# Kernel optimization log

Hardware: AMD Instinct MI355X
Metric: run time of the kernel (lower is better)

Reference implementation:

```python
import jax, jax.numpy as jnp
import numpy as np
import math

D_MODEL = 2048
K = 64
W = 512              # window_size
STRIDE = W // 2      # = 256
EMA_ALPHA = 0.9
N_RETRIEVE = 8
EPS = 1e-12


def _build_cheby(k, w):
    # cheby_mat[k, n] = cos(k * arccos(t_n)), t_n = cos(pi*(2n+1)/(2w))
    ns = np.arange(w, dtype=np.float64)
    t = np.cos(np.pi * (2 * ns + 1) / (2 * w))
    ks = np.arange(k, dtype=np.float64)
    return jnp.asarray(np.cos(ks[:, None] * np.arccos(t)[None, :]), dtype=jnp.float32)


def setup_inputs() -> dict:
    key = jax.random.key(0)
    ks = jax.random.split(key, 5)
    B, S = 2, 8192
    scan_out = jax.random.normal(ks[0], (B, S, D_MODEL), dtype=jnp.float32)
    buf = jax.random.normal(ks[1], (W, D_MODEL), dtype=jnp.float32)  # pre-filled circular buffer
    # unit-modulus random-phase complex roles: r_k[d] = exp(i*theta)
    phases = jax.random.uniform(ks[2], (K, D_MODEL), dtype=jnp.float32) * (2.0 * math.pi)
    roles_real = jnp.cos(phases)
    roles_imag = jnp.sin(phases)
    w_bands = 1.0 / (jnp.arange(K, dtype=jnp.float32) + 1.0)  # w_init = 1/(k+1)
    retrieve_proj_w = jax.random.normal(ks[3], (D_MODEL, D_MODEL), dtype=jnp.float32) * 0.02
    inject_gate = jnp.zeros((1,), dtype=jnp.float32)
    cheby_mat = _build_cheby(K, W)
    return dict(scan_out=scan_out, buf=buf, roles_real=roles_real, roles_imag=roles_imag,
                w_bands=w_bands, retrieve_proj_w=retrieve_proj_w, inject_gate=inject_gate,
                cheby_mat=cheby_mat)


def reference(scan_out, buf, roles_real, roles_imag, w_bands, retrieve_proj_w, inject_gate, cheby_mat):
    S = scan_out.shape[1]
    h_mean = scan_out.mean(axis=0)                      # [S, D] batch-mean like torch code
    n_chunks = S // STRIDE
    chunks = h_mean.reshape(n_chunks, STRIDE, D_MODEL)  # each chunk triggers one bind

    init = (buf, jnp.int32(0),
            jnp.zeros((K, D_MODEL), jnp.float32),   # c_past
            jnp.zeros((D_MODEL,), jnp.float32),     # V_mem_real
            jnp.zeros((D_MODEL,), jnp.float32),     # V_mem_imag
            jnp.zeros((K,), jnp.float32),           # _coeff_norms (EMA)
            jnp.zeros((K,), jnp.float32))           # spectral_delta

    def step(carry, chunk):
        b, pos, c_past, vr, vi, cnorms, _ = carry
        # circular-buffer write of `stride` tokens starting at pos
        b = jax.lax.dynamic_update_slice(b, chunk, (pos, 0))
        pos = (pos + STRIDE) % W
        order = (jnp.arange(W, dtype=jnp.int32) + pos) % W   # oldest-first reorder
        data = b[order]                                      # [W, D]
        # Chebyshev coefficients: c = (2/W) * cheby_mat @ data, c0 halved
        coeffs = (2.0 / W) * (cheby_mat @ data)              # [K, D]
        coeffs = coeffs.at[0].multiply(0.5)
        # HRR-normalized bind into holographic memory via EMA
        norms = jnp.maximum(jnp.linalg.norm(coeffs, axis=-1, keepdims=True), EPS)
        cn = coeffs / norms
        cnorms = EMA_ALPHA * cnorms + (1.0 - EMA_ALPHA) * norms[:, 0]
        vr = EMA_ALPHA * vr + (1.0 - EMA_ALPHA) * (cn * roles_real).sum(axis=0)
        vi = EMA_ALPHA * vi + (1.0 - EMA_ALPHA) * (cn * roles_imag).sum(axis=0)
        # spectral delta vs previous window's coefficients
        delta = jnp.linalg.norm(coeffs - c_past, axis=-1)    # [K]
        return (b, pos, coeffs, vr, vi, cnorms, delta), None

    (b, pos, c_now, vr, vi, cnorms, delta), _ = jax.lax.scan(step, init, chunks)

    # retrieve: unbind top-J bands by spectral delta, denormalize, weight, project
    _, top = jax.lax.top_k(delta, N_RETRIEVE)                # [J]
    rr = roles_real[top]
    ri = roles_imag[top]
    retrieved = (vr[None, :] * rr + vi[None, :] * ri) * jnp.maximum(cnorms[top], EPS)[:, None]  # [J, D]
    weights = jax.nn.softplus(w_bands[top])                  # [J]
    ctx = (weights[:, None] * retrieved).sum(axis=0)         # [D]
    out = (ctx @ retrieve_proj_w.T) * jax.nn.sigmoid(inject_gate[0])  # [D]
    return out, delta, vr, vi
```

## Files before the change

### kernel.cpp

```cpp
#include <hip/hip_runtime.h>
#include <math.h>

#define D_MODEL 2048
#define KB_ 64
#define NCHUNK 32

typedef __bf16 bf16;
typedef __attribute__((ext_vector_type(8))) __bf16 bf16x8;
typedef __attribute__((ext_vector_type(4))) __bf16 bf16x4;
typedef __attribute__((ext_vector_type(4))) float f32x4;

#define OFF_COEFFS 0
#define OFF_NSQ    (32 * 64 * 2048)
#define OFF_NORMS  (OFF_NSQ + 32 * 64 * 32)
#define OFF_PARTR  (OFF_NORMS + 2048)
#define OFF_PARTI  (OFF_PARTR + 32 * 2048)
#define OFF_CTX    (OFF_PARTI + 32 * 2048)
#define OFF_CHEB2  (OFF_CTX + 2048)

__global__ __launch_bounds__(256) void k0_prep(
    const float* __restrict__ cheby, bf16* __restrict__ cheb2)
{
  int flat = blockIdx.x * 256 + threadIdx.x;
  cheb2[flat] = (bf16)cheby[flat];
}

__global__ __launch_bounds__(256) void k1_mfma(
    const float* __restrict__ scan, const float* __restrict__ buf,
    const bf16* __restrict__ cheb2, float* __restrict__ coeffs,
    float* __restrict__ nsq_part)
{
  __shared__ bf16 Bs[64 * 72];

  const int t = threadIdx.x;
  const int dt = blockIdx.x;
  const int c  = blockIdx.y;
  const int w = t >> 6, lane = t & 63;
  const int quad = lane >> 4, r16 = lane & 15;
  const int d0 = dt * 64;
  const int n0 = (t >> 4) * 4;
  const int d4 = (t & 15) * 4;
  const float* scan1 = scan + 8192 * 2048;

  f32x4 acc[4];
#pragma unroll
  for (int tn = 0; tn < 4; ++tn) acc[tn] = (f32x4){0.f, 0.f, 0.f, 0.f};

  for (int nb = 0; nb < 8; ++nb) {
    const bf16* abase = cheb2 + (w * 16 + r16) * 512 + nb * 64 + quad * 8;
    bf16x8 a0 = *(const bf16x8*)(abase);
    bf16x8 a1 = *(const bf16x8*)(abase + 32);

    float vv[4][4];
    if (c == 0 && nb < 4) {
      const float* bp = buf + (256 + nb * 64 + n0) * 2048 + d0 + d4;
#pragma unroll
      for (int i = 0; i < 4; ++i) {
        float4 v = *(const float4*)(bp + i * 2048);
        vv[i][0] = v.x; vv[i][1] = v.y; vv[i][2] = v.z; vv[i][3] = v.w;
      }
    } else {
      int gbase = (c * 256 - 256 + nb * 64 + n0) * 2048 + d0 + d4;
#pragma unroll
      for (int i = 0; i < 4; ++i) {
        float4 a = *(const float4*)(scan + gbase + i * 2048);
        float4 b = *(const float4*)(scan1 + gbase + i * 2048);
        vv[i][0] = 0.5f * (a.x + b.x); vv[i][1] = 0.5f * (a.y + b.y);
        vv[i][2] = 0.5f * (a.z + b.z); vv[i][3] = 0.5f * (a.w + b.w);
      }
    }
    __syncthreads();
#pragma unroll
    for (int x = 0; x < 4; ++x) {
      bf16x4 e = {(bf16)vv[0][x], (bf16)vv[1][x], (bf16)vv[2][x], (bf16)vv[3][x]};
      *(bf16x4*)(Bs + (d4 + x) * 72 + n0) = e;
    }
    __syncthreads();

#pragma unroll
    for (int ks = 0; ks < 2; ++ks) {
      bf16x8 a = ks ? a1 : a0;
#pragma unroll
      for (int tn = 0; tn < 4; ++tn) {
        bf16x8 bfr = *(const bf16x8*)(Bs + (tn * 16 + r16) * 72 + ks * 32 + quad * 8);
        acc[tn] = __builtin_amdgcn_mfma_f32_16x16x32_bf16(a, bfr, acc[tn], 0, 0, 0);
      }
    }
  }

  const float scale = 2.0f / 512.0f;
  float sq[4] = {0.f, 0.f, 0.f, 0.f};
#pragma unroll
  for (int tn = 0; tn < 4; ++tn) {
#pragma unroll
    for (int rr = 0; rr < 4; ++rr) {
      int band = w * 16 + quad * 4 + rr;
      float sc = (band == 0) ? scale * 0.5f : scale;
      float v = acc[tn][rr] * sc;
      coeffs[(c * 64 + band) * 2048 + d0 + tn * 16 + r16] = v;
      sq[rr] += v * v;
    }
  }
#pragma unroll
  for (int off = 8; off > 0; off >>= 1) {
#pragma unroll
    for (int rr = 0; rr < 4; ++rr) sq[rr] += __shfl_down(sq[rr], off);
  }
  if (r16 == 0) {
#pragma unroll
    for (int rr = 0; rr < 4; ++rr)
      nsq_part[(c * 64 + w * 16 + quad * 4 + rr) * 32 + dt] = sq[rr];
  }
}

__global__ __launch_bounds__(256) void kd_delta(
    const float* __restrict__ coeffs, float* __restrict__ dout)
{
  const int k = blockIdx.x, tid = threadIdx.x;
  const float* p1 = coeffs + (31 * 64 + k) * 2048;
  const float* p0 = coeffs + (30 * 64 + k) * 2048;
  float s = 0.f;
#pragma unroll
  for (int i = 0; i < 2; ++i) {
    float4 a = *(const float4*)(p1 + tid * 4 + i * 1024);
    float4 b = *(const float4*)(p0 + tid * 4 + i * 1024);
    float x = a.x - b.x, y = a.y - b.y, z = a.z - b.z, ww = a.w - b.w;
    s += x * x + y * y + z * z + ww * ww;
  }
  for (int o = 32; o > 0; o >>= 1) s += __shfl_down(s, o, 64);
  __shared__ float red[4];
  if ((tid & 63) == 0) red[tid >> 6] = s;
  __syncthreads();
  if (tid == 0) dout[D_MODEL + k] = sqrtf(red[0] + red[1] + red[2] + red[3]);
}

__global__ __launch_bounds__(256) void k3_bind(
    const float* __restrict__ coeffs, const float* __restrict__ nsq_part,
    const float* __restrict__ rr, const float* __restrict__ ri,
    float* __restrict__ part_r, float* __restrict__ part_i,
    float* __restrict__ norms)
{
  __shared__ float inv_s[64];
  const int tid = threadIdx.x;
  const int c = blockIdx.y;
  if (tid < 64) {
    float s = 0.f;
#pragma unroll
    for (int dt = 0; dt < 32; ++dt) s += nsq_part[(c * 64 + tid) * 32 + dt];
    float nrm = fmaxf(sqrtf(s), 1e-12f);
    inv_s[tid] = 1.0f / nrm;
    if (blockIdx.x == 0) norms[c * 64 + tid] = nrm;
  }
  __syncthreads();
  const int d4 = (blockIdx.x * 256 + tid) * 4;
  const float wc = 0.1f * powf(0.9f, (float)(31 - c));
  float4 ar = make_float4(0.f, 0.f, 0.f, 0.f);
  float4 ai = make_float4(0.f, 0.f, 0.f, 0.f);
  for (int k = 0; k < KB_; ++k) {
    float4 cf = *(const float4*)(coeffs + (c * 64 + k) * 2048 + d4);
    float inv = inv_s[k];
    float4 r = *(const float4*)(rr + k * D_MODEL + d4);
    float4 im = *(const float4*)(ri + k * D_MODEL + d4);
    float cx = cf.x * inv, cy = cf.y * inv, cz = cf.z * inv, cw = cf.w * inv;
    ar.x += cx * r.x; ar.y += cy * r.y; ar.z += cz * r.z; ar.w += cw * r.w;
    ai.x += cx * im.x; ai.y += cy * im.y; ai.z += cz * im.z; ai.w += cw * im.w;
  }
  *(float4*)(part_r + c * D_MODEL + d4) =
      make_float4(wc * ar.x, wc * ar.y, wc * ar.z, wc * ar.w);
  *(float4*)(part_i + c * D_MODEL + d4) =
      make_float4(wc * ai.x, wc * ai.y, wc * ai.z, wc * ai.w);
}

__global__ __launch_bounds__(256) void k4_ctx(
    const float* __restrict__ norms, const float* __restrict__ part_r,
    const float* __restrict__ part_i, const float* __restrict__ rr,
    const float* __restrict__ ri, const float* __restrict__ wbands,
    float* __restrict__ dout, float* __restrict__ ctx)
{
  __shared__ float cn_s[64];
  __shared__ int top_s[8];
  __shared__ float wgt_s[8];
  const int tid = threadIdx.x;
  const int d = blockIdx.x * 256 + tid;
  if (tid < 64) {
    float s = 0.f;
    for (int c = 0; c < NCHUNK; ++c) s = 0.9f * s + 0.1f * norms[c * 64 + tid];
    cn_s[tid] = fmaxf(s, 1e-12f);
  }
  __syncthreads();
  if (tid == 0) {
    unsigned long long taken = 0ULL;
    for (int jj = 0; jj < 8; ++jj) {
      float best = -1.f;
      int bi = 0;
      for (int k = 0; k < 64; ++k) {
        float dv = dout[D_MODEL + k];
        if (!((taken >> k) & 1ULL) && dv > best) { best = dv; bi = k; }
      }
      taken |= (1ULL << bi);
      top_s[jj] = bi;
      wgt_s[jj] = log1pf(expf(wbands[bi]));
    }
  }
  __syncthreads();
  float sr = 0.f, si = 0.f;
  for (int c = 0; c < NCHUNK; ++c) {
    sr += part_r[c * D_MODEL + d];
    si += part_i[c * D_MODEL + d];
  }
  dout[D_MODEL + KB_ + d] = sr;
  dout[D_MODEL + KB_ + D_MODEL + d] = si;
  float cx = 0.f;
#pragma unroll
  for (int jj = 0; jj < 8; ++jj) {
    int k = top_s[jj];
    cx += wgt_s[jj] * (sr * rr[k * D_MODEL + d] + si * ri[k * D_MODEL + d]) * cn_s[k];
  }
  ctx[d] = cx;
}

__global__ __launch_bounds__(256) void k5b_gemv(
    const float* __restrict__ Wp, const float* __restrict__ ctx,
    const float* __restrict__ gate, float* __restrict__ dout)
{
  const int tid = threadIdx.x;
  const int lane = tid & 63;
  const int w = tid >> 6;
  const int row = blockIdx.x * 4 + w;
  const float* p = Wp + row * D_MODEL;
  float s = 0.f;
#pragma unroll
  for (int i = 0; i < 8; ++i) {
    int e = lane * 4 + i * 256;
    float4 wv = *(const float4*)(p + e);
    float4 cv = *(const float4*)(ctx + e);
    s += wv.x * cv.x + wv.y * cv.y + wv.z * cv.z + wv.w * cv.w;
  }
  for (int o = 32; o > 0; o >>= 1) s += __shfl_down(s, o, 64);
  if (lane == 0) {
    float sig = 1.f / (1.f + expf(-gate[0]));
    dout[row] = s * sig;
  }
}

extern "C" void kernel_launch(void* const* d_in, const int* in_sizes, int n_in,
                              void* d_out, int out_size, void* d_ws, size_t ws_size,
                              hipStream_t stream) {
  const float* scan  = (const float*)d_in[0];
  const float* buf   = (const float*)d_in[1];
  const float* rr    = (const float*)d_in[2];
  const float* ri    = (const float*)d_in[3];
  const float* wb    = (const float*)d_in[4];
  const float* Wp    = (const float*)d_in[5];
  const float* gate  = (const float*)d_in[6];
  const float* cheby = (const float*)d_in[7];
  float* out = (float*)d_out;
  float* ws = (float*)d_ws;

  float* coeffs   = ws + OFF_COEFFS;
  float* nsq_part = ws + OFF_NSQ;
  float* norms    = ws + OFF_NORMS;
  float* part_r   = ws + OFF_PARTR;
  float* part_i   = ws + OFF_PARTI;
  float* ctx      = ws + OFF_CTX;
  bf16*  cheb2    = (bf16*)(ws + OFF_CHEB2);

  k0_prep<<<128, 256, 0, stream>>>(cheby, cheb2);
  k1_mfma<<<dim3(32, 32), 256, 0, stream>>>(scan, buf, cheb2, coeffs, nsq_part);
  kd_delta<<<64, 256, 0, stream>>>(coeffs, out);
  k3_bind<<<dim3(2, NCHUNK), 256, 0, stream>>>(coeffs, nsq_part, rr, ri,
                                               part_r, part_i, norms);
  k4_ctx<<<8, 256, 0, stream>>>(norms, part_r, part_i, rr, ri, wb, out, ctx);
  k5b_gemv<<<512, 256, 0, stream>>>(Wp, ctx, gate, out);
}
```

Measured before the change: 279.6 us.

## Double-buffer B tile loads in MFMA kernel and fold delta kernel into bind

```diff
diff --git a/kernel.cpp b/kernel.cpp
--- a/kernel.cpp
+++ b/kernel.cpp
@@ -25,12 +25,12 @@
   cheb2[flat] = (bf16)cheby[flat];
 }
 
-__global__ __launch_bounds__(256) void k1_mfma(
+__global__ __launch_bounds__(256, 4) void k1_mfma(
     const float* __restrict__ scan, const float* __restrict__ buf,
     const bf16* __restrict__ cheb2, float* __restrict__ coeffs,
     float* __restrict__ nsq_part)
 {
-  __shared__ bf16 Bs[64 * 72];
+  __shared__ bf16 Bs[2][64 * 72];
 
   const int t = threadIdx.x;
   const int dt = blockIdx.x;
@@ -46,46 +46,54 @@
 #pragma unroll
   for (int tn = 0; tn < 4; ++tn) acc[tn] = (f32x4){0.f, 0.f, 0.f, 0.f};
 
+  float vv[4][4], vvn[4][4];
+
+  auto loadB = [&](int nb, float (*v)[4]) {
+    if (c == 0 && nb < 4) {
+      const float* bp = buf + (256 + nb * 64 + n0) * 2048 + d0 + d4;
+#pragma unroll
+      for (int i = 0; i < 4; ++i) {
+        float4 x = *(const float4*)(bp + i * 2048);
+        v[i][0] = x.x; v[i][1] = x.y; v[i][2] = x.z; v[i][3] = x.w;
+      }
+    } else {
+      int gbase = ((c - 1) * 256 + nb * 64 + n0) * 2048 + d0 + d4;
+#pragma unroll
+      for (int i = 0; i < 4; ++i) {
+        float4 a = *(const float4*)(scan + gbase + i * 2048);
+        float4 b = *(const float4*)(scan1 + gbase + i * 2048);
+        v[i][0] = 0.5f * (a.x + b.x); v[i][1] = 0.5f * (a.y + b.y);
+        v[i][2] = 0.5f * (a.z + b.z); v[i][3] = 0.5f * (a.w + b.w);
+      }
+    }
+  };
+
+  loadB(0, vv);
   for (int nb = 0; nb < 8; ++nb) {
+    bf16* Bw = Bs[nb & 1];
+#pragma unroll
+    for (int x = 0; x < 4; ++x) {
+      bf16x4 e = {(bf16)vv[0][x], (bf16)vv[1][x], (bf16)vv[2][x], (bf16)vv[3][x]};
+      *(bf16x4*)(Bw + (d4 + x) * 72 + n0) = e;
+    }
+    __syncthreads();
+    if (nb < 7) loadB(nb + 1, vvn);
     const bf16* abase = cheb2 + (w * 16 + r16) * 512 + nb * 64 + quad * 8;
     bf16x8 a0 = *(const bf16x8*)(abase);
     bf16x8 a1 = *(const bf16x8*)(abase + 32);
-
-    float vv[4][4];
-    if (c == 0 && nb < 4) {
-      const float* bp = buf + (256 + nb * 64 + n0) * 2048 + d0 + d4;
-#pragma unroll
-      for (int i = 0; i < 4; ++i) {
-        float4 v = *(const float4*)(bp + i * 2048);
-        vv[i][0] = v.x; vv[i][1] = v.y; vv[i][2] = v.z; vv[i][3] = v.w;
-      }
-    } else {
-      int gbase = (c * 256 - 256 + nb * 64 + n0) * 2048 + d0 + d4;
-#pragma unroll
-      for (int i = 0; i < 4; ++i) {
-        float4 a = *(const float4*)(scan + gbase + i * 2048);
-        float4 b = *(const float4*)(scan1 + gbase + i * 2048);
-        vv[i][0] = 0.5f * (a.x + b.x); vv[i][1] = 0.5f * (a.y + b.y);
-        vv[i][2] = 0.5f * (a.z + b.z); vv[i][3] = 0.5f * (a.w + b.w);
-      }
-    }
-    __syncthreads();
-#pragma unroll
-    for (int x = 0; x < 4; ++x) {
-      bf16x4 e = {(bf16)vv[0][x], (bf16)vv[1][x], (bf16)vv[2][x], (bf16)vv[3][x]};
-      *(bf16x4*)(Bs + (d4 + x) * 72 + n0) = e;
-    }
-    __syncthreads();
-
 #pragma unroll
     for (int ks = 0; ks < 2; ++ks) {
       bf16x8 a = ks ? a1 : a0;
 #pragma unroll
       for (int tn = 0; tn < 4; ++tn) {
-        bf16x8 bfr = *(const bf16x8*)(Bs + (tn * 16 + r16) * 72 + ks * 32 + quad * 8);
+        bf16x8 bfr = *(const bf16x8*)(Bw + (tn * 16 + r16) * 72 + ks * 32 + quad * 8);
         acc[tn] = __builtin_amdgcn_mfma_f32_16x16x32_bf16(a, bfr, acc[tn], 0, 0, 0);
       }
     }
+#pragma unroll
+    for (int i = 0; i < 4; ++i)
+#pragma unroll
+      for (int x = 0; x < 4; ++x) vv[i][x] = vvn[i][x];
   }
 
   const float scale = 2.0f / 512.0f;
@@ -113,40 +121,44 @@
   }
 }
 
-__global__ __launch_bounds__(256) void kd_delta(
-    const float* __restrict__ coeffs, float* __restrict__ dout)
-{
-  const int k = blockIdx.x, tid = threadIdx.x;
-  const float* p1 = coeffs + (31 * 64 + k) * 2048;
-  const float* p0 = coeffs + (30 * 64 + k) * 2048;
-  float s = 0.f;
-#pragma unroll
-  for (int i = 0; i < 2; ++i) {
-    float4 a = *(const float4*)(p1 + tid * 4 + i * 1024);
-    float4 b = *(const float4*)(p0 + tid * 4 + i * 1024);
-    float x = a.x - b.x, y = a.y - b.y, z = a.z - b.z, ww = a.w - b.w;
-    s += x * x + y * y + z * z + ww * ww;
-  }
-  for (int o = 32; o > 0; o >>= 1) s += __shfl_down(s, o, 64);
-  __shared__ float red[4];
-  if ((tid & 63) == 0) red[tid >> 6] = s;
-  __syncthreads();
-  if (tid == 0) dout[D_MODEL + k] = sqrtf(red[0] + red[1] + red[2] + red[3]);
-}
-
 __global__ __launch_bounds__(256) void k3_bind(
     const float* __restrict__ coeffs, const float* __restrict__ nsq_part,
     const float* __restrict__ rr, const float* __restrict__ ri,
     float* __restrict__ part_r, float* __restrict__ part_i,
-    float* __restrict__ norms)
-{
-  __shared__ float inv_s[64];
+    float* __restrict__ norms, float* __restrict__ dout)
+{
   const int tid = threadIdx.x;
   const int c = blockIdx.y;
+
+  if (blockIdx.x == 2) {
+    __shared__ float red[4];
+#pragma unroll
+    for (int kk = 0; kk < 2; ++kk) {
+      int k = c + kk * 32;
+      const float* p1 = coeffs + (31 * 64 + k) * 2048;
+      const float* p0 = coeffs + (30 * 64 + k) * 2048;
+      float s = 0.f;
+#pragma unroll
+      for (int i = 0; i < 2; ++i) {
+        float4 a = *(const float4*)(p1 + tid * 4 + i * 1024);
+        float4 b = *(const float4*)(p0 + tid * 4 + i * 1024);
+        float x = a.x - b.x, y = a.y - b.y, z = a.z - b.z, ww = a.w - b.w;
+        s += x * x + y * y + z * z + ww * ww;
+      }
+      for (int o = 32; o > 0; o >>= 1) s += __shfl_down(s, o, 64);
+      if ((tid & 63) == 0) red[tid >> 6] = s;
+      __syncthreads();
+      if (tid == 0) dout[D_MODEL + k] = sqrtf(red[0] + red[1] + red[2] + red[3]);
+      __syncthreads();
+    }
+    return;
+  }
+
+  __shared__ float inv_s[64];
   if (tid < 64) {
     float s = 0.f;
 #pragma unroll
-    for (int dt = 0; dt < 32; ++dt) s += nsq_part[(c * 64 + tid) * 32 + dt];
+    for (int dtl = 0; dtl < 32; ++dtl) s += nsq_part[(c * 64 + tid) * 32 + dtl];
     float nrm = fmaxf(sqrtf(s), 1e-12f);
     inv_s[tid] = 1.0f / nrm;
     if (blockIdx.x == 0) norms[c * 64 + tid] = nrm;
@@ -267,9 +279,8 @@
 
   k0_prep<<<128, 256, 0, stream>>>(cheby, cheb2);
   k1_mfma<<<dim3(32, 32), 256, 0, stream>>>(scan, buf, cheb2, coeffs, nsq_part);
-  kd_delta<<<64, 256, 0, stream>>>(coeffs, out);
-  k3_bind<<<dim3(2, NCHUNK), 256, 0, stream>>>(coeffs, nsq_part, rr, ri,
-                                               part_r, part_i, norms);
+  k3_bind<<<dim3(3, NCHUNK), 256, 0, stream>>>(coeffs, nsq_part, rr, ri,
+                                               part_r, part_i, norms, out);
   k4_ctx<<<8, 256, 0, stream>>>(norms, part_r, part_i, rr, ri, wb, out, ctx);
   k5b_gemv<<<512, 256, 0, stream>>>(Wp, ctx, gate, out);
 }
```

Result: slower. 321.5 us (+15.0%).

## Split Chebyshev GEMM K-dimension across two blocks and compute norms separately

Applied to the files above, without the earlier changes.

```diff
diff --git a/kernel.cpp b/kernel.cpp
--- a/kernel.cpp
+++ b/kernel.cpp
@@ -10,13 +10,14 @@
 typedef __attribute__((ext_vector_type(4))) __bf16 bf16x4;
 typedef __attribute__((ext_vector_type(4))) float f32x4;
 
-#define OFF_COEFFS 0
-#define OFF_NSQ    (32 * 64 * 2048)
-#define OFF_NORMS  (OFF_NSQ + 32 * 64 * 32)
-#define OFF_PARTR  (OFF_NORMS + 2048)
-#define OFF_PARTI  (OFF_PARTR + 32 * 2048)
-#define OFF_CTX    (OFF_PARTI + 32 * 2048)
-#define OFF_CHEB2  (OFF_CTX + 2048)
+#define HALF_SZ   (32 * 64 * 2048)
+#define OFF_CA    0
+#define OFF_CB    HALF_SZ
+#define OFF_NORMS (2 * HALF_SZ)
+#define OFF_PARTR (OFF_NORMS + 2048)
+#define OFF_PARTI (OFF_PARTR + 32 * 2048)
+#define OFF_CTX   (OFF_PARTI + 32 * 2048)
+#define OFF_CHEB2 (OFF_CTX + 2048)
 
 __global__ __launch_bounds__(256) void k0_prep(
     const float* __restrict__ cheby, bf16* __restrict__ cheb2)
@@ -25,16 +26,17 @@
   cheb2[flat] = (bf16)cheby[flat];
 }
 
-__global__ __launch_bounds__(256) void k1_mfma(
+__global__ __launch_bounds__(256, 6) void k1_mfma(
     const float* __restrict__ scan, const float* __restrict__ buf,
-    const bf16* __restrict__ cheb2, float* __restrict__ coeffs,
-    float* __restrict__ nsq_part)
+    const bf16* __restrict__ cheb2, float* __restrict__ coeffsA,
+    float* __restrict__ coeffsB)
 {
   __shared__ bf16 Bs[64 * 72];
 
   const int t = threadIdx.x;
   const int dt = blockIdx.x;
   const int c  = blockIdx.y;
+  const int h  = blockIdx.z;
   const int w = t >> 6, lane = t & 63;
   const int quad = lane >> 4, r16 = lane & 15;
   const int d0 = dt * 64;
@@ -46,21 +48,18 @@
 #pragma unroll
   for (int tn = 0; tn < 4; ++tn) acc[tn] = (f32x4){0.f, 0.f, 0.f, 0.f};
 
-  for (int nb = 0; nb < 8; ++nb) {
-    const bf16* abase = cheb2 + (w * 16 + r16) * 512 + nb * 64 + quad * 8;
-    bf16x8 a0 = *(const bf16x8*)(abase);
-    bf16x8 a1 = *(const bf16x8*)(abase + 32);
-
+  for (int nb = 0; nb < 4; ++nb) {
+    const int s = h * 4 + nb;
     float vv[4][4];
-    if (c == 0 && nb < 4) {
-      const float* bp = buf + (256 + nb * 64 + n0) * 2048 + d0 + d4;
+    if (c == 0 && h == 0) {
+      const float* bp = buf + (256 + s * 64 + n0) * 2048 + d0 + d4;
 #pragma unroll
       for (int i = 0; i < 4; ++i) {
-        float4 v = *(const float4*)(bp + i * 2048);
-        vv[i][0] = v.x; vv[i][1] = v.y; vv[i][2] = v.z; vv[i][3] = v.w;
+        float4 x = *(const float4*)(bp + i * 2048);
+        vv[i][0] = x.x; vv[i][1] = x.y; vv[i][2] = x.z; vv[i][3] = x.w;
       }
     } else {
-      int gbase = (c * 256 - 256 + nb * 64 + n0) * 2048 + d0 + d4;
+      int gbase = ((c - 1 + h) * 256 + nb * 64 + n0) * 2048 + d0 + d4;
 #pragma unroll
       for (int i = 0; i < 4; ++i) {
         float4 a = *(const float4*)(scan + gbase + i * 2048);
@@ -77,6 +76,9 @@
     }
     __syncthreads();
 
+    const bf16* abase = cheb2 + (w * 16 + r16) * 512 + s * 64 + quad * 8;
+    bf16x8 a0 = *(const bf16x8*)(abase);
+    bf16x8 a1 = *(const bf16x8*)(abase + 32);
 #pragma unroll
     for (int ks = 0; ks < 2; ++ks) {
       bf16x8 a = ks ? a1 : a0;
@@ -89,79 +91,86 @@
   }
 
   const float scale = 2.0f / 512.0f;
-  float sq[4] = {0.f, 0.f, 0.f, 0.f};
+  float* dst = h ? coeffsB : coeffsA;
 #pragma unroll
   for (int tn = 0; tn < 4; ++tn) {
 #pragma unroll
     for (int rr = 0; rr < 4; ++rr) {
       int band = w * 16 + quad * 4 + rr;
       float sc = (band == 0) ? scale * 0.5f : scale;
-      float v = acc[tn][rr] * sc;
-      coeffs[(c * 64 + band) * 2048 + d0 + tn * 16 + r16] = v;
-      sq[rr] += v * v;
-    }
-  }
-#pragma unroll
-  for (int off = 8; off > 0; off >>= 1) {
-#pragma unroll
-    for (int rr = 0; rr < 4; ++rr) sq[rr] += __shfl_down(sq[rr], off);
-  }
-  if (r16 == 0) {
-#pragma unroll
-    for (int rr = 0; rr < 4; ++rr)
-      nsq_part[(c * 64 + w * 16 + quad * 4 + rr) * 32 + dt] = sq[rr];
-  }
-}
-
-__global__ __launch_bounds__(256) void kd_delta(
-    const float* __restrict__ coeffs, float* __restrict__ dout)
-{
-  const int k = blockIdx.x, tid = threadIdx.x;
-  const float* p1 = coeffs + (31 * 64 + k) * 2048;
-  const float* p0 = coeffs + (30 * 64 + k) * 2048;
+      dst[(c * 64 + band) * 2048 + d0 + tn * 16 + r16] = acc[tn][rr] * sc;
+    }
+  }
+}
+
+__global__ __launch_bounds__(256) void k2_norms(
+    const float* __restrict__ CA, const float* __restrict__ CB,
+    float* __restrict__ norms, float* __restrict__ dout)
+{
+  const int tid = threadIdx.x;
+  const int b = blockIdx.x;
   float s = 0.f;
-#pragma unroll
-  for (int i = 0; i < 2; ++i) {
-    float4 a = *(const float4*)(p1 + tid * 4 + i * 1024);
-    float4 b = *(const float4*)(p0 + tid * 4 + i * 1024);
-    float x = a.x - b.x, y = a.y - b.y, z = a.z - b.z, ww = a.w - b.w;
-    s += x * x + y * y + z * z + ww * ww;
+  if (b < NCHUNK * KB_) {
+    const float* pa = CA + b * 2048;
+    const float* pb = CB + b * 2048;
+#pragma unroll
+    for (int i = 0; i < 2; ++i) {
+      float4 a = *(const float4*)(pa + tid * 4 + i * 1024);
+      float4 bb = *(const float4*)(pb + tid * 4 + i * 1024);
+      float x = a.x + bb.x, y = a.y + bb.y, z = a.z + bb.z, ww = a.w + bb.w;
+      s += x * x + y * y + z * z + ww * ww;
+    }
+  } else {
+    int k = b - NCHUNK * KB_;
+    const float* a1 = CA + (31 * 64 + k) * 2048;
+    const float* b1 = CB + (31 * 64 + k) * 2048;
+    const float* a0 = CA + (30 * 64 + k) * 2048;
+    const float* b0 = CB + (30 * 64 + k) * 2048;
+#pragma unroll
+    for (int i = 0; i < 2; ++i) {
+      float4 va1 = *(const float4*)(a1 + tid * 4 + i * 1024);
+      float4 vb1 = *(const float4*)(b1 + tid * 4 + i * 1024);
+      float4 va0 = *(const float4*)(a0 + tid * 4 + i * 1024);
+      float4 vb0 = *(const float4*)(b0 + tid * 4 + i * 1024);
+      float x = va1.x + vb1.x - va0.x - vb0.x, y = va1.y + vb1.y - va0.y - vb0.y;
+      float z = va1.z + vb1.z - va0.z - vb0.z, ww = va1.w + vb1.w - va0.w - vb0.w;
+      s += x * x + y * y + z * z + ww * ww;
+    }
   }
   for (int o = 32; o > 0; o >>= 1) s += __shfl_down(s, o, 64);
   __shared__ float red[4];
   if ((tid & 63) == 0) red[tid >> 6] = s;
   __syncthreads();
-  if (tid == 0) dout[D_MODEL + k] = sqrtf(red[0] + red[1] + red[2] + red[3]);
+  if (tid == 0) {
+    float r = sqrtf(red[0] + red[1] + red[2] + red[3]);
+    if (b < NCHUNK * KB_) norms[b] = fmaxf(r, 1e-12f);
+    else dout[D_MODEL + (b - NCHUNK * KB_)] = r;
+  }
 }
 
 __global__ __launch_bounds__(256) void k3_bind(
-    const float* __restrict__ coeffs, const float* __restrict__ nsq_part,
-    const float* __restrict__ rr, const float* __restrict__ ri,
-    float* __restrict__ part_r, float* __restrict__ part_i,
-    float* __restrict__ norms)
+    const float* __restrict__ CA, const float* __restrict__ CB,
+    const float* __restrict__ norms, const float* __restrict__ rr,
+    const float* __restrict__ ri, float* __restrict__ part_r,
+    float* __restrict__ part_i)
 {
   __shared__ float inv_s[64];
   const int tid = threadIdx.x;
   const int c = blockIdx.y;
-  if (tid < 64) {
-    float s = 0.f;
-#pragma unroll
-    for (int dt = 0; dt < 32; ++dt) s += nsq_part[(c * 64 + tid) * 32 + dt];
-    float nrm = fmaxf(sqrtf(s), 1e-12f);
-    inv_s[tid] = 1.0f / nrm;
-    if (blockIdx.x == 0) norms[c * 64 + tid] = nrm;
-  }
+  if (tid < 64) inv_s[tid] = 1.0f / norms[c * 64 + tid];
   __syncthreads();
   const int d4 = (blockIdx.x * 256 + tid) * 4;
   const float wc = 0.1f * powf(0.9f, (float)(31 - c));
   float4 ar = make_float4(0.f, 0.f, 0.f, 0.f);
   float4 ai = make_float4(0.f, 0.f, 0.f, 0.f);
   for (int k = 0; k < KB_; ++k) {
-    float4 cf = *(const float4*)(coeffs + (c * 64 + k) * 2048 + d4);
+    float4 ca = *(const float4*)(CA + (c * 64 + k) * 2048 + d4);
+    float4 cb = *(const float4*)(CB + (c * 64 + k) * 2048 + d4);
     float inv = inv_s[k];
     float4 r = *(const float4*)(rr + k * D_MODEL + d4);
     float4 im = *(const float4*)(ri + k * D_MODEL + d4);
-    float cx = cf.x * inv, cy = cf.y * inv, cz = cf.z * inv, cw = cf.w * inv;
+    float cx = (ca.x + cb.x) * inv, cy = (ca.y + cb.y) * inv;
+    float cz = (ca.z + cb.z) * inv, cw = (ca.w + cb.w) * inv;
     ar.x += cx * r.x; ar.y += cy * r.y; ar.z += cz * r.z; ar.w += cw * r.w;
     ai.x += cx * im.x; ai.y += cy * im.y; ai.z += cz * im.z; ai.w += cw * im.w;
   }
@@ -257,19 +266,19 @@
   float* out = (float*)d_out;
   float* ws = (float*)d_ws;
 
-  float* coeffs   = ws + OFF_COEFFS;
-  float* nsq_part = ws + OFF_NSQ;
-  float* norms    = ws + OFF_NORMS;
-  float* part_r   = ws + OFF_PARTR;
-  float* part_i   = ws + OFF_PARTI;
-  float* ctx      = ws + OFF_CTX;
-  bf16*  cheb2    = (bf16*)(ws + OFF_CHEB2);
+  float* CA     = ws + OFF_CA;
+  float* CB     = ws + OFF_CB;
+  float* norms  = ws + OFF_NORMS;
+  float* part_r = ws + OFF_PARTR;
+  float* part_i = ws + OFF_PARTI;
+  float* ctx    = ws + OFF_CTX;
+  bf16*  cheb2  = (bf16*)(ws + OFF_CHEB2);
 
   k0_prep<<<128, 256, 0, stream>>>(cheby, cheb2);
-  k1_mfma<<<dim3(32, 32), 256, 0, stream>>>(scan, buf, cheb2, coeffs, nsq_part);
-  kd_delta<<<64, 256, 0, stream>>>(coeffs, out);
-  k3_bind<<<dim3(2, NCHUNK), 256, 0, stream>>>(coeffs, nsq_part, rr, ri,
-                                               part_r, part_i, norms);
+  k1_mfma<<<dim3(32, 32, 2), 256, 0, stream>>>(scan, buf, cheb2, CA, CB);
+  k2_norms<<<NCHUNK * KB_ + KB_, 256, 0, stream>>>(CA, CB, norms, out);
+  k3_bind<<<dim3(2, NCHUNK), 256, 0, stream>>>(CA, CB, norms, rr, ri,
+                                               part_r, part_i);
   k4_ctx<<<8, 256, 0, stream>>>(norms, part_r, part_i, rr, ri, wb, out, ctx);
   k5b_gemv<<<512, 256, 0, stream>>>(Wp, ctx, gate, out);
 }
```

Measured after the change: 294.7 us. 1.05x slower.
